# Kernel optimization log

Hardware: AMD Instinct MI355X
Metric: run time of the kernel (lower is better)

## Reference

```python
import jax, jax.numpy as jnp
from jax import lax
import numpy as np


def setup_inputs() -> dict:
    key = jax.random.key(0)
    k1, k2, k3, k4 = jax.random.split(key, 4)
    B, T, D_in, D_out, M = 64, 512, 256, 1024, 8
    x = jax.random.normal(k1, (B, T, D_in), dtype=jnp.float32)
    # nn.Linear-style init scale (kept simple: scaled normal)
    W_in = jax.random.normal(k2, (D_in, D_out), dtype=jnp.float32) / np.sqrt(D_in)
    b_in = jax.random.normal(k3, (D_out,), dtype=jnp.float32) * 0.01
    W_h = jax.random.normal(k4, (D_out, D_out), dtype=jnp.float32) / np.sqrt(D_out)
    periods = jnp.ones((M,), dtype=jnp.float32)   # torch.zeros(M) + 1
    shifts = jnp.zeros((M,), dtype=jnp.float32)   # torch.zeros(M)
    return {"x": x, "W_in": W_in, "b_in": b_in, "W_h": W_h,
            "periods": periods, "shifts": shifts}


def reference(x, W_in, b_in, W_h, periods, shifts):
    B, T, D_in = x.shape
    D_out = W_in.shape[1]
    M = periods.shape[0]
    module_size = D_out // M

    def step(h, inp):
        ti, xi = inp                                  # ti scalar, xi [B, D_in]
        acts = jnp.tanh(xi @ W_in + b_in + h @ W_h)   # [B, D_out]
        gate_m = (jnp.sin(ti * periods + shifts) + 1.0) * 0.5  # [M]
        gate = jnp.repeat(gate_m, module_size)        # [D_out], per-module gate
        y = (1.0 - gate) * acts + gate * h
        return y, y

    h0 = jnp.zeros((B, D_out), dtype=x.dtype)
    ts = jnp.arange(T, dtype=x.dtype)
    h_final, ys = lax.scan(step, h0, (ts, jnp.swapaxes(x, 0, 1)))
    return jnp.swapaxes(ys, 0, 1), h_final  # ([B, T, D_out], [B, D_out])
```

## Files before the change

### kernel.cpp

```cpp
#include <hip/hip_runtime.h>

#define Bz   64
#define Tz   512
#define DIN  256
#define DOUT 1024
#define MODSZ 128

__global__ __launch_bounds__(256) void zgemm_kernel(
    const float* __restrict__ x, const float* __restrict__ Win,
    const float* __restrict__ bin, float* __restrict__ out)
{
    __shared__ float xT[32 * 132];
    __shared__ float ws[32 * 68];

    const int n0 = blockIdx.x * 128;
    const int c0 = blockIdx.y * 64;
    const int tid = threadIdx.x;
    const int tr = tid >> 4;
    const int tc = tid & 15;

    float acc[8][4];
#pragma unroll
    for (int i = 0; i < 8; ++i)
#pragma unroll
        for (int j = 0; j < 4; ++j) acc[i][j] = 0.f;

    for (int k0 = 0; k0 < DIN; k0 += 32) {
#pragma unroll
        for (int p = 0; p < 4; ++p) {
            int s = tid + p * 256;
            int r = s >> 3, kq = s & 7;
            float4 v = *(const float4*)(x + (size_t)(n0 + r) * DIN + k0 + kq * 4);
            xT[(kq * 4 + 0) * 132 + r] = v.x;
            xT[(kq * 4 + 1) * 132 + r] = v.y;
            xT[(kq * 4 + 2) * 132 + r] = v.z;
            xT[(kq * 4 + 3) * 132 + r] = v.w;
        }
#pragma unroll
        for (int p = 0; p < 2; ++p) {
            int s = tid + p * 256;
            int kk = s >> 4, cq = s & 15;
            *(float4*)(ws + kk * 68 + cq * 4) =
                *(const float4*)(Win + (size_t)(k0 + kk) * DOUT + c0 + cq * 4);
        }
        __syncthreads();
#pragma unroll
        for (int kk = 0; kk < 32; ++kk) {
            float4 a0 = *(const float4*)(xT + kk * 132 + tr * 4);
            float4 a1 = *(const float4*)(xT + kk * 132 + 64 + tr * 4);
            float4 b4 = *(const float4*)(ws + kk * 68 + tc * 4);
            float av[8] = {a0.x, a0.y, a0.z, a0.w, a1.x, a1.y, a1.z, a1.w};
            float bv[4] = {b4.x, b4.y, b4.z, b4.w};
#pragma unroll
            for (int i = 0; i < 8; ++i)
#pragma unroll
                for (int j = 0; j < 4; ++j)
                    acc[i][j] = fmaf(av[i], bv[j], acc[i][j]);
        }
        __syncthreads();
    }

    float4 bb = *(const float4*)(bin + c0 + tc * 4);
#pragma unroll
    for (int i = 0; i < 8; ++i) {
        int r = (i < 4) ? (tr * 4 + i) : (64 + tr * 4 + (i - 4));
        float4 o;
        o.x = acc[i][0] + bb.x;
        o.y = acc[i][1] + bb.y;
        o.z = acc[i][2] + bb.z;
        o.w = acc[i][3] + bb.w;
        *(float4*)(out + (size_t)(n0 + r) * DOUT + c0 + tc * 4) = o;
    }
}

__device__ __forceinline__ int hswz(int r, int idx) {
    return idx ^ r ^ ((idx >> 4) & 48);
}

__global__ __launch_bounds__(256) void step_kernel(
    int t, const float* __restrict__ h_in, float* __restrict__ h_out,
    const float* __restrict__ Wh, const float* __restrict__ periods,
    const float* __restrict__ shifts, float* __restrict__ out)
{
    __shared__ float hs[16 * 1024];

    const int cg = blockIdx.x & 63;
    const int rg = blockIdx.x >> 6;
    const int c0 = cg * 16;
    const int r0 = rg * 16;
    const int tid = threadIdx.x;

    {
        const int row = tid >> 4;
        const int sb  = tid & 15;
#pragma unroll
        for (int i = 0; i < 16; ++i) {
            int s = sb + i * 16;
            float4 v = *(const float4*)(h_in + (size_t)(r0 + row) * DOUT + s * 4);
            int base = row * 1024;
            hs[base + hswz(row, s * 4 + 0)] = v.x;
            hs[base + hswz(row, s * 4 + 1)] = v.y;
            hs[base + hswz(row, s * 4 + 2)] = v.z;
            hs[base + hswz(row, s * 4 + 3)] = v.w;
        }
    }
    __syncthreads();

    const int cq   = tid & 3;
    const int half = (tid >> 2) & 3;
    const int r    = tid >> 4;
    const int c    = c0 + cq * 4;
    const int k0h  = half * 256;
    const float* wp = Wh + c;
    const float* hp = hs + r * 1024;

    float a0 = 0.f, a1 = 0.f, a2 = 0.f, a3 = 0.f;
#pragma unroll 16
    for (int k = 0; k < 256; ++k) {
        int kk = k0h + k;
        float4 w4 = *(const float4*)(wp + (size_t)kk * DOUT);
        float hv = hp[hswz(r, kk)];
        a0 = fmaf(hv, w4.x, a0);
        a1 = fmaf(hv, w4.y, a1);
        a2 = fmaf(hv, w4.z, a2);
        a3 = fmaf(hv, w4.w, a3);
    }
    a0 += __shfl_xor(a0, 4); a0 += __shfl_xor(a0, 8);
    a1 += __shfl_xor(a1, 4); a1 += __shfl_xor(a1, 8);
    a2 += __shfl_xor(a2, 4); a2 += __shfl_xor(a2, 8);
    a3 += __shfl_xor(a3, 4); a3 += __shfl_xor(a3, 8);

    if (half == 0) {
        const int m = c >> 7;
        const float g  = 0.5f * (sinf((float)t * periods[m] + shifts[m]) + 1.0f);
        const float og = 1.0f - g;

        const size_t zidx = (size_t)(r0 + r) * ((size_t)Tz * DOUT) + (size_t)t * DOUT + c;
        float4 z4 = *(const float4*)(out + zidx);
        float h0 = hp[hswz(r, c + 0)];
        float h1 = hp[hswz(r, c + 1)];
        float h2 = hp[hswz(r, c + 2)];
        float h3 = hp[hswz(r, c + 3)];
        float4 y;
        y.x = og * tanhf(z4.x + a0) + g * h0;
        y.y = og * tanhf(z4.y + a1) + g * h1;
        y.z = og * tanhf(z4.z + a2) + g * h2;
        y.w = og * tanhf(z4.w + a3) + g * h3;
        *(float4*)(out + zidx) = y;
        *(float4*)(h_out + (size_t)(r0 + r) * DOUT + c) = y;
        if (t == Tz - 1)
            *(float4*)(out + (size_t)Bz * Tz * DOUT + (size_t)(r0 + r) * DOUT + c) = y;
    }
}

extern "C" void kernel_launch(void* const* d_in, const int* in_sizes, int n_in,
                              void* d_out, int out_size, void* d_ws, size_t ws_size,
                              hipStream_t stream)
{
    const float* x   = (const float*)d_in[0];
    const float* Win = (const float*)d_in[1];
    const float* bin = (const float*)d_in[2];
    const float* Wh  = (const float*)d_in[3];
    const float* per = (const float*)d_in[4];
    const float* shf = (const float*)d_in[5];
    float* out = (float*)d_out;

    float* ha = (float*)d_ws;
    float* hb = ha + (size_t)Bz * DOUT;

    hipMemsetAsync(ha, 0, (size_t)Bz * DOUT * sizeof(float), stream);
    zgemm_kernel<<<dim3(256, 16), 256, 0, stream>>>(x, Win, bin, out);
    for (int t = 0; t < Tz; ++t) {
        step_kernel<<<256, 256, 0, stream>>>(t, ha, hb, Wh, per, shf, out);
        float* tmp = ha; ha = hb; hb = tmp;
    }
}
```

Before: 5.864 ms.

## Replace per-timestep kernel launches with persistent cooperative kernel using grid sync

```diff
diff --git a/kernel.cpp b/kernel.cpp
--- a/kernel.cpp
+++ b/kernel.cpp
@@ -1,10 +1,15 @@
 #include <hip/hip_runtime.h>
+#include <hip/hip_cooperative_groups.h>
+
+namespace cg = cooperative_groups;
 
 #define Bz   64
 #define Tz   512
 #define DIN  256
 #define DOUT 1024
-#define MODSZ 128
+#define NWG  256
+#define NTHR 512
+#define PSTR 272
 
 __global__ __launch_bounds__(256) void zgemm_kernel(
     const float* __restrict__ x, const float* __restrict__ Win,
@@ -73,6 +78,148 @@
     }
 }
 
+__global__ __launch_bounds__(512, 1) void cwrnn_persistent(
+    const float* __restrict__ Wh, const float* __restrict__ periods,
+    const float* __restrict__ shifts, float* __restrict__ out)
+{
+    extern __shared__ float lds[];
+    float* Whs = lds;
+    float* hls = lds + 16384;
+    float* P   = hls;
+
+    cg::grid_group grid = cg::this_grid();
+
+    const int bid = blockIdx.x;
+    const int tid = threadIdx.x;
+    const int r0 = (bid >> 6) * 16;
+    const int c0 = (bid & 63) * 16;
+
+    {
+        const int cq4 = tid & 3, kb = tid >> 2;
+#pragma unroll
+        for (int p = 0; p < 8; ++p) {
+            int k = p * 128 + kb;
+            *(float4*)(Whs + k * 16 + cq4 * 4) =
+                *(const float4*)(Wh + (size_t)k * DOUT + c0 + cq4 * 4);
+        }
+    }
+    __syncthreads();
+
+    const bool owner = (tid < 256);
+    const int orow = tid >> 4;
+    const int occ  = tid & 15;
+    const int oc   = c0 + occ;
+    float pm = 0.f, sm = 0.f;
+    if (owner) { pm = periods[oc >> 7]; sm = shifts[oc >> 7]; }
+
+    const int cq = tid & 3;
+    const int rq = (tid >> 2) & 3;
+    const int ks = tid >> 4;
+
+    const int srow = tid >> 5;
+    const int skc  = tid & 31;
+
+    for (int t = 0; t < Tz; ++t) {
+        float zval = 0.f;
+        const size_t zoff = (size_t)(r0 + orow) * ((size_t)Tz * DOUT)
+                          + (size_t)t * DOUT + oc;
+        if (owner) zval = out[zoff];
+
+        float acc[4][4];
+#pragma unroll
+        for (int i = 0; i < 4; ++i)
+#pragma unroll
+            for (int j = 0; j < 4; ++j) acc[i][j] = 0.f;
+
+        float hprev = 0.f;
+
+        if (t > 0) {
+            {
+                const float* src = out
+                    + (size_t)(r0 + srow) * ((size_t)Tz * DOUT)
+                    + (size_t)(t - 1) * DOUT;
+                float tmp[32];
+#pragma unroll
+                for (int i = 0; i < 32; ++i)
+                    tmp[i] = __hip_atomic_load(src + i * 32 + skc,
+                                               __ATOMIC_RELAXED,
+                                               __HIP_MEMORY_SCOPE_SYSTEM);
+                float* dst = hls + srow * 1024;
+#pragma unroll
+                for (int i = 0; i < 32; ++i)
+                    dst[i * 32 + skc] = tmp[i];
+            }
+            __syncthreads();
+
+            {
+                const float* h0 = hls + (rq * 4 + 0) * 1024;
+                const float* h1 = hls + (rq * 4 + 1) * 1024;
+                const float* h2 = hls + (rq * 4 + 2) * 1024;
+                const float* h3 = hls + (rq * 4 + 3) * 1024;
+#pragma unroll
+                for (int p = 0; p < 8; ++p) {
+                    const int kb = p * 128 + ks * 4;
+                    float4 w0 = *(const float4*)(Whs + (kb + 0) * 16 + cq * 4);
+                    float4 w1 = *(const float4*)(Whs + (kb + 1) * 16 + cq * 4);
+                    float4 w2 = *(const float4*)(Whs + (kb + 2) * 16 + cq * 4);
+                    float4 w3 = *(const float4*)(Whs + (kb + 3) * 16 + cq * 4);
+                    float4 ha = *(const float4*)(h0 + kb);
+                    float4 hb = *(const float4*)(h1 + kb);
+                    float4 hc = *(const float4*)(h2 + kb);
+                    float4 hd = *(const float4*)(h3 + kb);
+                    float hv[4][4] = {
+                        {ha.x, ha.y, ha.z, ha.w}, {hb.x, hb.y, hb.z, hb.w},
+                        {hc.x, hc.y, hc.z, hc.w}, {hd.x, hd.y, hd.z, hd.w}};
+                    float4 wv[4] = {w0, w1, w2, w3};
+#pragma unroll
+                    for (int j = 0; j < 4; ++j)
+#pragma unroll
+                        for (int i = 0; i < 4; ++i) {
+                            acc[i][0] = fmaf(hv[i][j], wv[j].x, acc[i][0]);
+                            acc[i][1] = fmaf(hv[i][j], wv[j].y, acc[i][1]);
+                            acc[i][2] = fmaf(hv[i][j], wv[j].z, acc[i][2]);
+                            acc[i][3] = fmaf(hv[i][j], wv[j].w, acc[i][3]);
+                        }
+                }
+            }
+            __syncthreads();
+            if (owner) hprev = hls[orow * 1024 + oc];
+            __syncthreads();
+        }
+
+        {
+            float* pp = P + ks * PSTR + rq * 68 + cq * 4;
+#pragma unroll
+            for (int i = 0; i < 4; ++i) {
+                pp[i * 16 + 0] = acc[i][0];
+                pp[i * 16 + 1] = acc[i][1];
+                pp[i * 16 + 2] = acc[i][2];
+                pp[i * 16 + 3] = acc[i][3];
+            }
+        }
+        __syncthreads();
+
+        if (owner) {
+            const float* pp = P + (orow >> 2) * 68 + (orow & 3) * 16 + occ;
+            float sum = 0.f;
+#pragma unroll
+            for (int s = 0; s < 32; ++s) sum += pp[s * PSTR];
+            float a = tanhf(zval + sum);
+            float g = 0.5f * (sinf((float)t * pm + sm) + 1.0f);
+            float y = (1.0f - g) * a + g * hprev;
+            __hip_atomic_store(out + zoff, y, __ATOMIC_RELAXED,
+                               __HIP_MEMORY_SCOPE_SYSTEM);
+            if (t == Tz - 1)
+                out[(size_t)Bz * Tz * DOUT + (size_t)(r0 + orow) * DOUT + oc] = y;
+        }
+
+        if (t != Tz - 1) {
+            __syncthreads();
+            grid.sync();
+        }
+    }
+}
+
 __device__ __forceinline__ int hswz(int r, int idx) {
     return idx ^ r ^ ((idx >> 4) & 48);
 }
@@ -84,9 +231,9 @@
 {
     __shared__ float hs[16 * 1024];
 
-    const int cg = blockIdx.x & 63;
+    const int cg_ = blockIdx.x & 63;
     const int rg = blockIdx.x >> 6;
-    const int c0 = cg * 16;
+    const int c0 = cg_ * 16;
     const int r0 = rg * 16;
     const int tid = threadIdx.x;
 
@@ -165,13 +312,28 @@
     const float* shf = (const float*)d_in[5];
     float* out = (float*)d_out;
 
-    float* ha = (float*)d_ws;
-    float* hb = ha + (size_t)Bz * DOUT;
-
-    hipMemsetAsync(ha, 0, (size_t)Bz * DOUT * sizeof(float), stream);
     zgemm_kernel<<<dim3(256, 16), 256, 0, stream>>>(x, Win, bin, out);
-    for (int t = 0; t < Tz; ++t) {
-        step_kernel<<<256, 256, 0, stream>>>(t, ha, hb, Wh, per, shf, out);
-        float* tmp = ha; ha = hb; hb = tmp;
-    }
-}
+
+    const int ldsBytes = 131072;
+
+    bool coop_ok = false;
+    hipError_t err = hipFuncSetAttribute((const void*)cwrnn_persistent,
+                        hipFuncAttributeMaxDynamicSharedMemorySize, ldsBytes);
+    if (err == hipSuccess) {
+        void* args[] = { (void*)&Wh, (void*)&per, (void*)&shf, (void*)&out };
+        err = hipLaunchCooperativeKernel((const void*)cwrnn_persistent,
+                                         dim3(NWG), dim3(NTHR), args,
+                                         ldsBytes, stream);
+        coop_ok = (err == hipSuccess);
+    }
+
+    if (!coop_ok) {
+        float* ha = (float*)d_ws;
+        float* hb = ha + (size_t)Bz * DOUT;
+        hipMemsetAsync(ha, 0, (size_t)Bz * DOUT * sizeof(float), stream);
+        for (int t = 0; t < Tz; ++t) {
+            step_kernel<<<256, 256, 0, stream>>>(t, ha, hb, Wh, per, shf, out);
+            float* tmp = ha; ha = hb; hb = tmp;
+        }
+    }
+}
```

After: 12.03 ms. 2.05x slower.
